# Optimization experiments

Hardware: AMD Instinct MI355X
Metric: run time of the kernel (lower is better)

The kernel has to match this reference:

```python
import jax, jax.numpy as jnp
import numpy as np

N_FEATURES = 3072
LATENT_DIM = 128
BATCH = 8192


def setup_inputs() -> dict:
    key = jax.random.key(0)
    k1, k2, k3, k4 = jax.random.split(key, 4)
    example = jax.random.normal(k1, (BATCH, N_FEATURES), dtype=jnp.float32)
    # small-ish W so C = W W^T + sigma^2 I is well conditioned
    W = jax.random.normal(k2, (N_FEATURES, LATENT_DIM), dtype=jnp.float32) * 0.05
    log_var = jax.random.normal(k3, (1,), dtype=jnp.float32) * 0.1
    training_mean = jax.random.normal(k4, (N_FEATURES,), dtype=jnp.float32)
    return {"example": example, "W": W, "log_var": log_var, "training_mean": training_mean}


def reference(example, W, log_var, training_mean):
    n = W.shape[0]
    # C = W W^T + exp(log_var) * I   -- [n, n] covariance, as in the original
    C = W @ W.T + jnp.exp(log_var[0]) * jnp.eye(n, dtype=W.dtype)
    _, logdetC = jnp.linalg.slogdet(C)
    precision = jnp.linalg.inv(C)
    res = example.reshape(-1, n) - training_mean.reshape(1, n)  # [B, n]
    # diag(res @ precision @ res^T) computed directly, avoiding the BxB matrix
    quad = jnp.einsum("bi,ij,bj->b", res, precision, res)  # [B]
    log_2pi = np.log(2.0 * np.pi).astype(np.float32)
    log_like = -0.5 * (n * log_2pi + logdetC + quad)  # [B]
    return log_like
```

## Files before the change

### kernel.cpp

```cpp
#include <hip/hip_runtime.h>
#include <hip/hip_bf16.h>

#define N_FEAT 3072
#define LATENT 128
#define LOG2PI 1.8378770664093453f

typedef __attribute__((ext_vector_type(8))) short short8;
typedef __attribute__((ext_vector_type(4))) float f32x4;

__device__ __forceinline__ unsigned short f2bf(float x) {
  unsigned int u = __float_as_uint(x);
  u += 0x7FFFu + ((u >> 16) & 1u);
  return (unsigned short)(u >> 16);
}

typedef __attribute__((address_space(1))) const void gas_void;
typedef __attribute__((address_space(3))) void las_void;
__device__ __forceinline__ void gld_lds16(const void* g, void* s) {
  __builtin_amdgcn_global_load_lds((gas_void*)g, (las_void*)s, 16, 0, 0);
}

#define GR_CHUNK 64
__global__ __launch_bounds__(256) void k_prep(const float* __restrict__ W,
                                              float* __restrict__ Mp,
                                              unsigned short* __restrict__ Wt) {
  __shared__ __align__(16) float Ws[GR_CHUNK * 128];
  int t = threadIdx.x;
  int k0 = blockIdx.x * GR_CHUNK;
  const float* src = W + (size_t)k0 * 128;
#pragma unroll
  for (int c = 0; c < 8; ++c)
    ((float4*)Ws)[t + 256 * c] = ((const float4*)src)[t + 256 * c];
  __syncthreads();
  int tr = t >> 4, tc = t & 15;
  float acc[8][8];
#pragma unroll
  for (int r = 0; r < 8; ++r)
#pragma unroll
    for (int c = 0; c < 8; ++c) acc[r][c] = 0.f;
#pragma unroll 2
  for (int k = 0; k < GR_CHUNK; ++k) {
    f32x4 a0 = *(f32x4*)&Ws[k * 128 + 8 * tr];
    f32x4 a1 = *(f32x4*)&Ws[k * 128 + 8 * tr + 4];
    f32x4 b0 = *(f32x4*)&Ws[k * 128 + 8 * tc];
    f32x4 b1 = *(f32x4*)&Ws[k * 128 + 8 * tc + 4];
    float av[8] = {a0.x, a0.y, a0.z, a0.w, a1.x, a1.y, a1.z, a1.w};
    float bv[8] = {b0.x, b0.y, b0.z, b0.w, b1.x, b1.y, b1.z, b1.w};
#pragma unroll
    for (int r = 0; r < 8; ++r)
#pragma unroll
      for (int c = 0; c < 8; ++c) acc[r][c] = fmaf(av[r], bv[c], acc[r][c]);
  }
  float* dst = Mp + (size_t)blockIdx.x * 16384 + (size_t)(8 * tr) * 128 + 8 * tc;
#pragma unroll
  for (int r = 0; r < 8; ++r) {
    *(f32x4*)(dst + r * 128) = (f32x4){acc[r][0], acc[r][1], acc[r][2], acc[r][3]};
    *(f32x4*)(dst + r * 128 + 4) = (f32x4){acc[r][4], acc[r][5], acc[r][6], acc[r][7]};
  }
  int n = t >> 1, h = t & 1;
  unsigned pk[16];
#pragma unroll
  for (int c = 0; c < 16; ++c)
    pk[c] = (unsigned)f2bf(Ws[(h * 32 + 2 * c) * 128 + n]) |
            ((unsigned)f2bf(Ws[(h * 32 + 2 * c + 1) * 128 + n]) << 16);
  uint4* wd = (uint4*)(Wt + (size_t)n * N_FEAT + k0 + h * 32);
#pragma unroll
  for (int c = 0; c < 4; ++c)
    wd[c] = make_uint4(pk[4 * c], pk[4 * c + 1], pk[4 * c + 2], pk[4 * c + 3]);
}

__global__ __launch_bounds__(256) void k_red(const float* __restrict__ Mp,
                                             float* __restrict__ M) {
  int i = blockIdx.x * 256 + threadIdx.x;
  float s = 0.f;
#pragma unroll
  for (int p = 0; p < 48; ++p) s += Mp[(size_t)p * 16384 + i];
  M[i] = s;
}

__global__ __launch_bounds__(512, 4) void k_gemm(
    const float* __restrict__ ex, const float* __restrict__ mean,
    const unsigned short* __restrict__ Wt, float* __restrict__ M,
    float* __restrict__ scal, const float* __restrict__ log_var,
    float* __restrict__ Tp, float* __restrict__ sqp, int direct) {
  __shared__ __align__(16) unsigned short As[2][32][128];
  __shared__ __align__(16) unsigned short Bs[2][128][128];
  int t = threadIdx.x;

  if (blockIdx.x == 0) {
    float* sh = (float*)&As[0][0][0];
    float* PR = sh;
    float* PC = sh + 256;
    float* DB = sh + 512;
    float* DG = sh + 514;
    float* RD = sh + 642;
    bool act = t < 256;
    int itr = t >> 4, itc = t & 15;
    float lv = log_var[0];
    float sig2 = expf(lv);
    float a[8][8];
    if (act) {
      const float* srcM = M + (size_t)(8 * itr) * 128 + 8 * itc;
#pragma unroll
      for (int r = 0; r < 8; ++r) {
        f32x4 v0 = *(const f32x4*)(srcM + r * 128);
        f32x4 v1 = *(const f32x4*)(srcM + r * 128 + 4);
        a[r][0] = v0.x; a[r][1] = v0.y; a[r][2] = v0.z; a[r][3] = v0.w;
        a[r][4] = v1.x; a[r][5] = v1.y; a[r][6] = v1.z; a[r][7] = v1.w;
      }
      if (itr == itc) {
#pragma unroll
        for (int r = 0; r < 8; ++r) a[r][r] += sig2;
      }
      if (itr == 0) {
#pragma unroll
        for (int c = 0; c < 8; ++c) PR[8 * itc + c] = a[0][c];
      }
      if (itc == 0) {
#pragma unroll
        for (int r = 0; r < 8; ++r) PC[8 * itr + r] = a[r][0];
      }
      if (t == 0) DB[0] = a[0][0];
    }
    __syncthreads();
    for (int kb = 0; kb < 16; ++kb) {
#pragma unroll
      for (int lk = 0; lk < 8; ++lk) {
        const int k = kb * 8 + lk;
        const int buf = k & 1;
        if (act) {
          float d = DB[buf];
          if (t == 0) DG[k] = d;
          float p = 1.0f / d;
          float pr[8], pc[8];
#pragma unroll
          for (int c = 0; c < 8; ++c) pr[c] = PR[buf * 128 + 8 * itc + c] * p;
#pragma unroll
          for (int r = 0; r < 8; ++r) pc[r] = PC[buf * 128 + 8 * itr + r];
#pragma unroll
          for (int r = 0; r < 8; ++r)
#pragma unroll
            for (int c = 0; c < 8; ++c) a[r][c] = fmaf(-pc[r], pr[c], a[r][c]);
          bool myrow = (itr == (k >> 3));
          bool mycol = (itc == (k >> 3));
          if (myrow) {
#pragma unroll
            for (int c = 0; c < 8; ++c) a[lk][c] = pr[c];
          }
          if (mycol) {
#pragma unroll
            for (int r = 0; r < 8; ++r) a[r][lk] = -p * pc[r];
          }
          if (myrow && mycol) a[lk][lk] = p;
          if (k + 1 < 128) {
            const int nb = buf ^ 1;
            const int nl = (lk + 1) & 7;
            const int nr = (k + 1) >> 3;
            if (itr == nr) {
#pragma unroll
              for (int c = 0; c < 8; ++c) PR[nb * 128 + 8 * itc + c] = a[nl][c];
            }
            if (itc == nr) {
#pragma unroll
              for (int r = 0; r < 8; ++r) PC[nb * 128 + 8 * itr + r] = a[r][nl];
            }
            if (itr == nr && itc == nr) DB[nb] = a[nl][nl];
          }
        }
        __syncthreads();
      }
    }
    if (act) {
      float* dst = M + (size_t)(8 * itr) * 128 + 8 * itc;
#pragma unroll
      for (int r = 0; r < 8; ++r) {
        f32x4 v0 = {a[r][0], a[r][1], a[r][2], a[r][3]};
        f32x4 v1 = {a[r][4], a[r][5], a[r][6], a[r][7]};
        *(f32x4*)(dst + r * 128) = v0;
        *(f32x4*)(dst + r * 128 + 4) = v1;
      }
    }
    float ld = 0.f;
    if (t < 128) ld = logf(DG[t]);
#pragma unroll
    for (int o = 1; o < 64; o <<= 1) ld += __shfl_xor(ld, o);
    if (t == 0) RD[0] = ld;
    if (t == 64) RD[1] = ld;
    __syncthreads();
    if (t == 0) {
      scal[0] = -0.5f * (N_FEAT * LOG2PI + (float)(N_FEAT - LATENT) * lv +
                         (RD[0] + RD[1]));
      scal[1] = expf(-lv);
    }
    return;
  }

  int gid = (int)blockIdx.x - 1;
  int half = gid >> 8;
  int rg = gid & 255;
  int r0 = rg * 32;
  const bool dual = (gid == 255);
  const int NT = dual ? 24 : 12;
  const int tg0 = dual ? 0 : half * 12;

  int lane = t & 63, w = t >> 6;

  int arow = t >> 4, ag = t & 15;
  const float* ep = ex + (size_t)(r0 + arow) * N_FEAT + (size_t)tg0 * 128 + ag * 8;
  const float* mp = mean + (size_t)tg0 * 128 + ag * 8;
  int awoff = arow * 256 + ((ag & 8) + ((ag + arow) & 7)) * 16;

  int sp = lane & 15, rl = lane >> 4;
  const unsigned short* bsrc[4];
#pragma unroll
  for (int j = 0; j < 4; ++j) {
    int n = w * 16 + j * 4 + rl;
    int s = (sp & 8) | ((sp - n) & 7);
    bsrc[j] = Wt + (size_t)n * N_FEAT + (size_t)tg0 * 128 + s * 8;
  }
  char* ldsB0 = (char*)Bs + (size_t)w * 4096;
  char* ldsB1 = (char*)Bs + 32768 + (size_t)w * 4096;

  int fr = lane & 15, fq = lane >> 4;
  int aoff0[4], aoff1[4], boff[4];
#pragma unroll
  for (int kk = 0; kk < 4; ++kk) {
    int sI = kk * 4 + fq;
    aoff0[kk] = fr * 256 + ((sI & 8) + ((sI + fr) & 7)) * 16;
    int ar1 = 16 + fr;
    aoff1[kk] = ar1 * 256 + ((sI & 8) + ((sI + ar1) & 7)) * 16;
    int n = w * 16 + fr;
    boff[kk] = n * 256 + ((sI & 8) + ((sI + n) & 7)) * 16;
  }

  f32x4 acc0 = {0.f, 0.f, 0.f, 0.f}, acc1 = {0.f, 0.f, 0.f, 0.f};
  float sq = 0.f;
  float4 e, e2, m, m2;

  auto issueA = [&](int it) {
    const float* p = ep + (size_t)it * 128;
    const float* q = mp + (size_t)it * 128;
    e  = *(const float4*)p;       e2 = *(const float4*)(p + 4);
    m  = *(const float4*)q;       m2 = *(const float4*)(q + 4);
  };
  auto issueB = [&](int it, int bufN) {
    char* d = bufN ? ldsB1 : ldsB0;
#pragma unroll
    for (int j = 0; j < 4; ++j)
      gld_lds16(bsrc[j] + (size_t)it * 128, d + j * 1024);
  };
  auto packA = [&](int bufN) {
    float r0_ = e.x - m.x,   r1_ = e.y - m.y,   r2_ = e.z - m.z,   r3_ = e.w - m.w;
    float r4_ = e2.x - m2.x, r5_ = e2.y - m2.y, r6_ = e2.z - m2.z, r7_ = e2.w - m2.w;
    sq = fmaf(r0_, r0_, sq); sq = fmaf(r1_, r1_, sq);
    sq = fmaf(r2_, r2_, sq); sq = fmaf(r3_, r3_, sq);
    sq = fmaf(r4_, r4_, sq); sq = fmaf(r5_, r5_, sq);
    sq = fmaf(r6_, r6_, sq); sq = fmaf(r7_, r7_, sq);
    uint4 pa;
    pa.x = (unsigned)f2bf(r0_) | ((unsigned)f2bf(r1_) << 16);
    pa.y = (unsigned)f2bf(r2_) | ((unsigned)f2bf(r3_) << 16);
    pa.z = (unsigned)f2bf(r4_) | ((unsigned)f2bf(r5_) << 16);
    pa.w = (unsigned)f2bf(r6_) | ((unsigned)f2bf(r7_) << 16);
    *(uint4*)((char*)As + bufN * 8192 + awoff) = pa;
  };
  auto mma = [&](int bufN) {
    char* Ab = (char*)As + bufN * 8192;
    char* Bb = (char*)Bs + bufN * 32768;
#pragma unroll
    for (int kk = 0; kk < 4; ++kk) {
      short8 a0 = *(const short8*)(Ab + aoff0[kk]);
      short8 a1 = *(const short8*)(Ab + aoff1[kk]);
      short8 b  = *(const short8*)(Bb + boff[kk]);
      acc0 = __builtin_amdgcn_mfma_f32_16x16x32_bf16(a0, b, acc0, 0, 0, 0);
      acc1 = __builtin_amdgcn_mfma_f32_16x16x32_bf16(a1, b, acc1, 0, 0, 0);
    }
  };

  issueA(0);
  __builtin_amdgcn_sched_barrier(0);
  issueB(0, 0);
  packA(0);
  asm volatile("s_waitcnt lgkmcnt(0)" ::: "memory");
  __builtin_amdgcn_s_barrier();
  __builtin_amdgcn_sched_barrier(0);

  for (int it = 0; it < NT - 1; ++it) {
    const int buf = it & 1;
    issueA(it + 1);
    __builtin_amdgcn_sched_barrier(0);
    issueB(it + 1, buf ^ 1);
    asm volatile("s_waitcnt vmcnt(8)" ::: "memory");
    __builtin_amdgcn_sched_barrier(0);
    mma(buf);
    packA(buf ^ 1);
    asm volatile("s_waitcnt lgkmcnt(0)" ::: "memory");
    __builtin_amdgcn_s_barrier();
    __builtin_amdgcn_sched_barrier(0);
  }
  asm volatile("s_waitcnt vmcnt(0)" ::: "memory");
  __builtin_amdgcn_sched_barrier(0);
  mma((NT - 1) & 1);

  sq += __shfl_xor(sq, 1); sq += __shfl_xor(sq, 2);
  sq += __shfl_xor(sq, 4); sq += __shfl_xor(sq, 8);

  if (direct) {
    if (ag == 0) sqp[half * 8192 + r0 + arow] = sq;
    float* tp = Tp + (size_t)half * 1048576 +
                (size_t)(r0 + fq * 4) * 128 + w * 16 + fr;
#pragma unroll
    for (int ii = 0; ii < 4; ++ii) {
      tp[(size_t)ii * 128] = acc0[ii];
      tp[(size_t)ii * 128 + 2048] = acc1[ii];
    }
    if (dual) {
      float* z = Tp + 1048576 + (size_t)r0 * 128;
      for (int i = t; i < 1024; i += 512) ((f32x4*)z)[i] = (f32x4){0, 0, 0, 0};
      if (t < 32) sqp[8192 + r0 + t] = 0.f;
    }
  } else {
    if (ag == 0) atomicAdd(&sqp[r0 + arow], sq);
    float* tp = Tp + (size_t)(r0 + fq * 4) * 128 + w * 16 + fr;
#pragma unroll
    for (int ii = 0; ii < 4; ++ii) {
      atomicAdd(tp + (size_t)ii * 128, acc0[ii]);
      atomicAdd(tp + (size_t)ii * 128 + 2048, acc1[ii]);
    }
  }
}

__global__ __launch_bounds__(256) void k_epi(const float* __restrict__ Tp,
                                             const float* __restrict__ sqp,
                                             const float* __restrict__ Minv,
                                             const float* __restrict__ scal,
                                             float* __restrict__ out, int two) {
  __shared__ __align__(16) float Ts[32][132];
  __shared__ float rs[32];
  int t = threadIdx.x;
  int r0 = blockIdx.x * 32;
  int sr = t >> 3, sseg = t & 7;
  const float* tp0 = Tp + (size_t)(r0 + sr) * 128 + sseg * 16;
#pragma unroll
  for (int c = 0; c < 4; ++c) {
    float4 v0 = *(const float4*)(tp0 + c * 4);
    if (two) {
      float4 v1 = *(const float4*)(tp0 + 1048576 + c * 4);
      v0.x += v1.x; v0.y += v1.y; v0.z += v1.z; v0.w += v1.w;
    }
    *(f32x4*)&Ts[sr][sseg * 16 + c * 4] = (f32x4){v0.x, v0.y, v0.z, v0.w};
  }
  if (t < 32) rs[t] = two ? (sqp[r0 + t] + sqp[8192 + r0 + t]) : sqp[r0 + t];
  __syncthreads();

  int rp = t >> 4, cg = t & 15;
  int ra = 2 * rp, rb = ra + 1;
  int c0 = cg * 8;
  float ya[8] = {0, 0, 0, 0, 0, 0, 0, 0};
  float yb[8] = {0, 0, 0, 0, 0, 0, 0, 0};
#pragma unroll 4
  for (int j = 0; j < 128; ++j) {
    float tav = Ts[ra][j];
    float tbv = Ts[rb][j];
    float4 v0 = *(const float4*)(Minv + j * LATENT + c0);
    float4 v1 = *(const float4*)(Minv + j * LATENT + c0 + 4);
    ya[0] = fmaf(tav, v0.x, ya[0]); ya[1] = fmaf(tav, v0.y, ya[1]);
    ya[2] = fmaf(tav, v0.z, ya[2]); ya[3] = fmaf(tav, v0.w, ya[3]);
    ya[4] = fmaf(tav, v1.x, ya[4]); ya[5] = fmaf(tav, v1.y, ya[5]);
    ya[6] = fmaf(tav, v1.z, ya[6]); ya[7] = fmaf(tav, v1.w, ya[7]);
    yb[0] = fmaf(tbv, v0.x, yb[0]); yb[1] = fmaf(tbv, v0.y, yb[1]);
    yb[2] = fmaf(tbv, v0.z, yb[2]); yb[3] = fmaf(tbv, v0.w, yb[3]);
    yb[4] = fmaf(tbv, v1.x, yb[4]); yb[5] = fmaf(tbv, v1.y, yb[5]);
    yb[6] = fmaf(tbv, v1.z, yb[6]); yb[7] = fmaf(tbv, v1.w, yb[7]);
  }
  float q0 = 0.f, q1 = 0.f;
#pragma unroll
  for (int c = 0; c < 8; ++c) {
    q0 = fmaf(ya[c], Ts[ra][c0 + c], q0);
    q1 = fmaf(yb[c], Ts[rb][c0 + c], q1);
  }
  q0 += __shfl_xor(q0, 1); q0 += __shfl_xor(q0, 2);
  q0 += __shfl_xor(q0, 4); q0 += __shfl_xor(q0, 8);
  q1 += __shfl_xor(q1, 1); q1 += __shfl_xor(q1, 2);
  q1 += __shfl_xor(q1, 4); q1 += __shfl_xor(q1, 8);
  if (cg == 0) {
    float cc = scal[0], is2 = scal[1];
    out[r0 + ra] = cc - 0.5f * is2 * (rs[ra] - q0);
    out[r0 + rb] = cc - 0.5f * is2 * (rs[rb] - q1);
  }
}

extern "C" void kernel_launch(void* const* d_in, const int* in_sizes, int n_in,
                              void* d_out, int out_size, void* d_ws, size_t ws_size,
                              hipStream_t stream) {
  (void)in_sizes; (void)n_in; (void)out_size;
  const float* ex   = (const float*)d_in[0];
  const float* W    = (const float*)d_in[1];
  const float* lv   = (const float*)d_in[2];
  const float* mean = (const float*)d_in[3];
  float* out = (float*)d_out;

  const size_t need_direct = (size_t)(16384 + 64 + 2097152 + 16384 + 196608) * 4;
  int direct = (ws_size >= need_direct) ? 1 : 0;

  float* M = (float*)d_ws;
  float* scal = M + 16384;
  float* Tp = scal + 64;
  float* sqp;
  unsigned short* Wt;
  if (direct) {
    sqp = Tp + 2097152;
    Wt = (unsigned short*)(sqp + 16384);
  } else {
    sqp = Tp + 1048576;
    Wt = (unsigned short*)(sqp + 8192);
  }
  float* Mp = Tp;

  k_prep<<<48, 256, 0, stream>>>(W, Mp, Wt);
  k_red<<<64, 256, 0, stream>>>(Mp, M);
  if (!direct)
    hipMemsetAsync(Tp, 0, (size_t)(1048576 + 8192) * sizeof(float), stream);
  k_gemm<<<512, 512, 0, stream>>>(ex, mean, Wt, M, scal, lv, Tp, sqp, direct);
  k_epi<<<256, 256, 0, stream>>>(Tp, sqp, M, scal, out, direct ? 1 : 0);
}
```

Baseline: 212.7 us.

## Fuse all stages into one cooperative kernel with grid syncs and split-K A pipelining

Merges the prep, reduction, inverse/GEMM and epilogue kernels into a single cooperative launch that separates stages with grid-wide barriers, removing per-launch overheads and gaps between kernels. The GEMM main loop is also restructured into a manually unrolled two-stage register pipeline for the activation loads. The dual-half special block is dropped, since block 0 now does the inverse and then the last row-group half. Separate-kernel fallbacks are kept for when the cooperative launch fails. The risks are grid.sync cost across 512 blocks and the occupancy needed for a cooperative launch of 512x512 threads.

```diff
diff --git a/kernel.cpp b/kernel.cpp
--- a/kernel.cpp
+++ b/kernel.cpp
@@ -1,5 +1,8 @@
 #include <hip/hip_runtime.h>
 #include <hip/hip_bf16.h>
+#include <hip/hip_cooperative_groups.h>
+
+namespace cg = cooperative_groups;
 
 #define N_FEAT 3072
 #define LATENT 128
@@ -20,189 +23,183 @@
   __builtin_amdgcn_global_load_lds((gas_void*)g, (las_void*)s, 16, 0, 0);
 }
 
-#define GR_CHUNK 64
-__global__ __launch_bounds__(256) void k_prep(const float* __restrict__ W,
-                                              float* __restrict__ Mp,
-                                              unsigned short* __restrict__ Wt) {
-  __shared__ __align__(16) float Ws[GR_CHUNK * 128];
-  int t = threadIdx.x;
-  int k0 = blockIdx.x * GR_CHUNK;
-  const float* src = W + (size_t)k0 * 128;
-#pragma unroll
-  for (int c = 0; c < 8; ++c)
-    ((float4*)Ws)[t + 256 * c] = ((const float4*)src)[t + 256 * c];
+__device__ void prep_body(char* smem, int bid, int t, const float* W,
+                          float* Mp, unsigned short* Wt) {
+  float* Ws = (float*)smem;
+  int k0 = bid * 64;
+  if (t < 256) {
+    const float* src = W + (size_t)k0 * 128;
+#pragma unroll
+    for (int c = 0; c < 8; ++c)
+      ((float4*)Ws)[t + 256 * c] = ((const float4*)src)[t + 256 * c];
+  }
   __syncthreads();
-  int tr = t >> 4, tc = t & 15;
-  float acc[8][8];
-#pragma unroll
-  for (int r = 0; r < 8; ++r)
-#pragma unroll
-    for (int c = 0; c < 8; ++c) acc[r][c] = 0.f;
+  if (t < 256) {
+    int tr = t >> 4, tc = t & 15;
+    float acc[8][8];
+#pragma unroll
+    for (int r = 0; r < 8; ++r)
+#pragma unroll
+      for (int c = 0; c < 8; ++c) acc[r][c] = 0.f;
 #pragma unroll 2
-  for (int k = 0; k < GR_CHUNK; ++k) {
-    f32x4 a0 = *(f32x4*)&Ws[k * 128 + 8 * tr];
-    f32x4 a1 = *(f32x4*)&Ws[k * 128 + 8 * tr + 4];
-    f32x4 b0 = *(f32x4*)&Ws[k * 128 + 8 * tc];
-    f32x4 b1 = *(f32x4*)&Ws[k * 128 + 8 * tc + 4];
-    float av[8] = {a0.x, a0.y, a0.z, a0.w, a1.x, a1.y, a1.z, a1.w};
-    float bv[8] = {b0.x, b0.y, b0.z, b0.w, b1.x, b1.y, b1.z, b1.w};
-#pragma unroll
-    for (int r = 0; r < 8; ++r)
-#pragma unroll
-      for (int c = 0; c < 8; ++c) acc[r][c] = fmaf(av[r], bv[c], acc[r][c]);
-  }
-  float* dst = Mp + (size_t)blockIdx.x * 16384 + (size_t)(8 * tr) * 128 + 8 * tc;
-#pragma unroll
-  for (int r = 0; r < 8; ++r) {
-    *(f32x4*)(dst + r * 128) = (f32x4){acc[r][0], acc[r][1], acc[r][2], acc[r][3]};
-    *(f32x4*)(dst + r * 128 + 4) = (f32x4){acc[r][4], acc[r][5], acc[r][6], acc[r][7]};
-  }
-  int n = t >> 1, h = t & 1;
-  unsigned pk[16];
-#pragma unroll
-  for (int c = 0; c < 16; ++c)
-    pk[c] = (unsigned)f2bf(Ws[(h * 32 + 2 * c) * 128 + n]) |
-            ((unsigned)f2bf(Ws[(h * 32 + 2 * c + 1) * 128 + n]) << 16);
-  uint4* wd = (uint4*)(Wt + (size_t)n * N_FEAT + k0 + h * 32);
-#pragma unroll
-  for (int c = 0; c < 4; ++c)
-    wd[c] = make_uint4(pk[4 * c], pk[4 * c + 1], pk[4 * c + 2], pk[4 * c + 3]);
-}
-
-__global__ __launch_bounds__(256) void k_red(const float* __restrict__ Mp,
-                                             float* __restrict__ M) {
-  int i = blockIdx.x * 256 + threadIdx.x;
-  float s = 0.f;
-#pragma unroll
-  for (int p = 0; p < 48; ++p) s += Mp[(size_t)p * 16384 + i];
-  M[i] = s;
-}
-
-__global__ __launch_bounds__(512, 4) void k_gemm(
-    const float* __restrict__ ex, const float* __restrict__ mean,
-    const unsigned short* __restrict__ Wt, float* __restrict__ M,
-    float* __restrict__ scal, const float* __restrict__ log_var,
-    float* __restrict__ Tp, float* __restrict__ sqp, int direct) {
-  __shared__ __align__(16) unsigned short As[2][32][128];
-  __shared__ __align__(16) unsigned short Bs[2][128][128];
-  int t = threadIdx.x;
-
-  if (blockIdx.x == 0) {
-    float* sh = (float*)&As[0][0][0];
-    float* PR = sh;
-    float* PC = sh + 256;
-    float* DB = sh + 512;
-    float* DG = sh + 514;
-    float* RD = sh + 642;
-    bool act = t < 256;
-    int itr = t >> 4, itc = t & 15;
-    float lv = log_var[0];
-    float sig2 = expf(lv);
-    float a[8][8];
-    if (act) {
-      const float* srcM = M + (size_t)(8 * itr) * 128 + 8 * itc;
-#pragma unroll
-      for (int r = 0; r < 8; ++r) {
-        f32x4 v0 = *(const f32x4*)(srcM + r * 128);
-        f32x4 v1 = *(const f32x4*)(srcM + r * 128 + 4);
-        a[r][0] = v0.x; a[r][1] = v0.y; a[r][2] = v0.z; a[r][3] = v0.w;
-        a[r][4] = v1.x; a[r][5] = v1.y; a[r][6] = v1.z; a[r][7] = v1.w;
+    for (int k = 0; k < 64; ++k) {
+      f32x4 a0 = *(f32x4*)&Ws[k * 128 + 8 * tr];
+      f32x4 a1 = *(f32x4*)&Ws[k * 128 + 8 * tr + 4];
+      f32x4 b0 = *(f32x4*)&Ws[k * 128 + 8 * tc];
+      f32x4 b1 = *(f32x4*)&Ws[k * 128 + 8 * tc + 4];
+      float av[8] = {a0.x, a0.y, a0.z, a0.w, a1.x, a1.y, a1.z, a1.w};
+      float bv[8] = {b0.x, b0.y, b0.z, b0.w, b1.x, b1.y, b1.z, b1.w};
+#pragma unroll
+      for (int r = 0; r < 8; ++r)
+#pragma unroll
+        for (int c = 0; c < 8; ++c) acc[r][c] = fmaf(av[r], bv[c], acc[r][c]);
+    }
+    float* dst = Mp + (size_t)bid * 16384 + (size_t)(8 * tr) * 128 + 8 * tc;
+#pragma unroll
+    for (int r = 0; r < 8; ++r) {
+      *(f32x4*)(dst + r * 128) =
+          (f32x4){acc[r][0], acc[r][1], acc[r][2], acc[r][3]};
+      *(f32x4*)(dst + r * 128 + 4) =
+          (f32x4){acc[r][4], acc[r][5], acc[r][6], acc[r][7]};
+    }
+    int n = t >> 1, h = t & 1;
+    unsigned pk[16];
+#pragma unroll
+    for (int c = 0; c < 16; ++c)
+      pk[c] = (unsigned)f2bf(Ws[(h * 32 + 2 * c) * 128 + n]) |
+              ((unsigned)f2bf(Ws[(h * 32 + 2 * c + 1) * 128 + n]) << 16);
+    uint4* wd = (uint4*)(Wt + (size_t)n * N_FEAT + k0 + h * 32);
+#pragma unroll
+    for (int c = 0; c < 4; ++c)
+      wd[c] = make_uint4(pk[4 * c], pk[4 * c + 1], pk[4 * c + 2], pk[4 * c + 3]);
+  }
+}
+
+__device__ void red_body(int bid, int t, const float* Mp, float* M) {
+  if (bid < 64 && t < 256) {
+    int i = bid * 256 + t;
+    float s = 0.f;
+#pragma unroll
+    for (int p = 0; p < 48; ++p) s += Mp[(size_t)p * 16384 + i];
+    M[i] = s;
+  }
+}
+
+__device__ void inverse_body(char* smem, int t, float* M, float* scal,
+                             const float* log_var) {
+  float* sh = (float*)smem;
+  float* PR = sh;
+  float* PC = sh + 256;
+  float* DB = sh + 512;
+  float* DG = sh + 514;
+  float* RD = sh + 642;
+  bool act = t < 256;
+  int itr = t >> 4, itc = t & 15;
+  float lv = log_var[0];
+  float sig2 = expf(lv);
+  float a[8][8];
+  if (act) {
+    const float* srcM = M + (size_t)(8 * itr) * 128 + 8 * itc;
+#pragma unroll
+    for (int r = 0; r < 8; ++r) {
+      f32x4 v0 = *(const f32x4*)(srcM + r * 128);
+      f32x4 v1 = *(const f32x4*)(srcM + r * 128 + 4);
+      a[r][0] = v0.x; a[r][1] = v0.y; a[r][2] = v0.z; a[r][3] = v0.w;
+      a[r][4] = v1.x; a[r][5] = v1.y; a[r][6] = v1.z; a[r][7] = v1.w;
+    }
+    if (itr == itc) {
+#pragma unroll
+      for (int r = 0; r < 8; ++r) a[r][r] += sig2;
+    }
+    if (itr == 0) {
+#pragma unroll
+      for (int c = 0; c < 8; ++c) PR[8 * itc + c] = a[0][c];
+    }
+    if (itc == 0) {
+#pragma unroll
+      for (int r = 0; r < 8; ++r) PC[8 * itr + r] = a[r][0];
+    }
+    if (t == 0) DB[0] = a[0][0];
+  }
+  __syncthreads();
+  for (int kb = 0; kb < 16; ++kb) {
+#pragma unroll
+    for (int lk = 0; lk < 8; ++lk) {
+      const int k = kb * 8 + lk;
+      const int buf = k & 1;
+      if (act) {
+        float d = DB[buf];
+        if (t == 0) DG[k] = d;
+        float p = 1.0f / d;
+        float pr[8], pc[8];
+#pragma unroll
+        for (int c = 0; c < 8; ++c) pr[c] = PR[buf * 128 + 8 * itc + c] * p;
+#pragma unroll
+        for (int r = 0; r < 8; ++r) pc[r] = PC[buf * 128 + 8 * itr + r];
+#pragma unroll
+        for (int r = 0; r < 8; ++r)
+#pragma unroll
+          for (int c = 0; c < 8; ++c) a[r][c] = fmaf(-pc[r], pr[c], a[r][c]);
+        bool myrow = (itr == (k >> 3));
+        bool mycol = (itc == (k >> 3));
+        if (myrow) {
+#pragma unroll
+          for (int c = 0; c < 8; ++c) a[lk][c] = pr[c];
+        }
+        if (mycol) {
+#pragma unroll
+          for (int r = 0; r < 8; ++r) a[r][lk] = -p * pc[r];
+        }
+        if (myrow && mycol) a[lk][lk] = p;
+        if (k + 1 < 128) {
+          const int nb = buf ^ 1;
+          const int nl = (lk + 1) & 7;
+          const int nr = (k + 1) >> 3;
+          if (itr == nr) {
+#pragma unroll
+            for (int c = 0; c < 8; ++c) PR[nb * 128 + 8 * itc + c] = a[nl][c];
+          }
+          if (itc == nr) {
+#pragma unroll
+            for (int r = 0; r < 8; ++r) PC[nb * 128 + 8 * itr + r] = a[r][nl];
+          }
+          if (itr == nr && itc == nr) DB[nb] = a[nl][nl];
+        }
       }
-      if (itr == itc) {
-#pragma unroll
-        for (int r = 0; r < 8; ++r) a[r][r] += sig2;
-      }
-      if (itr == 0) {
-#pragma unroll
-        for (int c = 0; c < 8; ++c) PR[8 * itc + c] = a[0][c];
-      }
-      if (itc == 0) {
-#pragma unroll
-        for (int r = 0; r < 8; ++r) PC[8 * itr + r] = a[r][0];
-      }
-      if (t == 0) DB[0] = a[0][0];
-    }
-    __syncthreads();
-    for (int kb = 0; kb < 16; ++kb) {
-#pragma unroll
-      for (int lk = 0; lk < 8; ++lk) {
-        const int k = kb * 8 + lk;
-        const int buf = k & 1;
-        if (act) {
-          float d = DB[buf];
-          if (t == 0) DG[k] = d;
-          float p = 1.0f / d;
-          float pr[8], pc[8];
-#pragma unroll
-          for (int c = 0; c < 8; ++c) pr[c] = PR[buf * 128 + 8 * itc + c] * p;
-#pragma unroll
-          for (int r = 0; r < 8; ++r) pc[r] = PC[buf * 128 + 8 * itr + r];
-#pragma unroll
-          for (int r = 0; r < 8; ++r)
-#pragma unroll
-            for (int c = 0; c < 8; ++c) a[r][c] = fmaf(-pc[r], pr[c], a[r][c]);
-          bool myrow = (itr == (k >> 3));
-          bool mycol = (itc == (k >> 3));
-          if (myrow) {
-#pragma unroll
-            for (int c = 0; c < 8; ++c) a[lk][c] = pr[c];
-          }
-          if (mycol) {
-#pragma unroll
-            for (int r = 0; r < 8; ++r) a[r][lk] = -p * pc[r];
-          }
-          if (myrow && mycol) a[lk][lk] = p;
-          if (k + 1 < 128) {
-            const int nb = buf ^ 1;
-            const int nl = (lk + 1) & 7;
-            const int nr = (k + 1) >> 3;
-            if (itr == nr) {
-#pragma unroll
-              for (int c = 0; c < 8; ++c) PR[nb * 128 + 8 * itc + c] = a[nl][c];
-            }
-            if (itc == nr) {
-#pragma unroll
-              for (int r = 0; r < 8; ++r) PC[nb * 128 + 8 * itr + r] = a[r][nl];
-            }
-            if (itr == nr && itc == nr) DB[nb] = a[nl][nl];
-          }
-        }
-        __syncthreads();
-      }
-    }
-    if (act) {
-      float* dst = M + (size_t)(8 * itr) * 128 + 8 * itc;
-#pragma unroll
-      for (int r = 0; r < 8; ++r) {
-        f32x4 v0 = {a[r][0], a[r][1], a[r][2], a[r][3]};
-        f32x4 v1 = {a[r][4], a[r][5], a[r][6], a[r][7]};
-        *(f32x4*)(dst + r * 128) = v0;
-        *(f32x4*)(dst + r * 128 + 4) = v1;
-      }
-    }
-    float ld = 0.f;
-    if (t < 128) ld = logf(DG[t]);
-#pragma unroll
-    for (int o = 1; o < 64; o <<= 1) ld += __shfl_xor(ld, o);
-    if (t == 0) RD[0] = ld;
-    if (t == 64) RD[1] = ld;
-    __syncthreads();
-    if (t == 0) {
-      scal[0] = -0.5f * (N_FEAT * LOG2PI + (float)(N_FEAT - LATENT) * lv +
-                         (RD[0] + RD[1]));
-      scal[1] = expf(-lv);
-    }
-    return;
-  }
-
-  int gid = (int)blockIdx.x - 1;
-  int half = gid >> 8;
-  int rg = gid & 255;
+      __syncthreads();
+    }
+  }
+  if (act) {
+    float* dst = M + (size_t)(8 * itr) * 128 + 8 * itc;
+#pragma unroll
+    for (int r = 0; r < 8; ++r) {
+      f32x4 v0 = {a[r][0], a[r][1], a[r][2], a[r][3]};
+      f32x4 v1 = {a[r][4], a[r][5], a[r][6], a[r][7]};
+      *(f32x4*)(dst + r * 128) = v0;
+      *(f32x4*)(dst + r * 128 + 4) = v1;
+    }
+  }
+  float ld = 0.f;
+  if (t < 128) ld = logf(DG[t]);
+#pragma unroll
+  for (int o = 1; o < 64; o <<= 1) ld += __shfl_xor(ld, o);
+  if (t == 0) RD[0] = ld;
+  if (t == 64) RD[1] = ld;
+  __syncthreads();
+  if (t == 0) {
+    scal[0] = -0.5f * (N_FEAT * LOG2PI + (float)(N_FEAT - LATENT) * lv +
+                       (RD[0] + RD[1]));
+    scal[1] = expf(-lv);
+  }
+}
+
+__device__ void gemm_body(char* smem, int rg, int half, int t,
+                          const float* ex, const float* mean,
+                          const unsigned short* Wt, float* Tp, float* sqp) {
+  char* As = smem;
+  char* Bs = smem + 16384;
   int r0 = rg * 32;
-  const bool dual = (gid == 255);
-  const int NT = dual ? 24 : 12;
-  const int tg0 = dual ? 0 : half * 12;
-
+  int tg0 = half * 12;
   int lane = t & 63, w = t >> 6;
 
   int arow = t >> 4, ag = t & 15;
@@ -218,8 +215,8 @@
     int s = (sp & 8) | ((sp - n) & 7);
     bsrc[j] = Wt + (size_t)n * N_FEAT + (size_t)tg0 * 128 + s * 8;
   }
-  char* ldsB0 = (char*)Bs + (size_t)w * 4096;
-  char* ldsB1 = (char*)Bs + 32768 + (size_t)w * 4096;
+  char* ldsB0 = Bs + (size_t)w * 4096;
+  char* ldsB1 = Bs + 32768 + (size_t)w * 4096;
 
   int fr = lane & 15, fq = lane >> 4;
   int aoff0[4], aoff1[4], boff[4];
@@ -235,21 +232,23 @@
 
   f32x4 acc0 = {0.f, 0.f, 0.f, 0.f}, acc1 = {0.f, 0.f, 0.f, 0.f};
   float sq = 0.f;
-  float4 e, e2, m, m2;
-
-  auto issueA = [&](int it) {
+  float4 eA, eA2, mA, mA2;
+  float4 eB, eB2, mB, mB2;
+
+  auto loadS0 = [&](int it) {
     const float* p = ep + (size_t)it * 128;
     const float* q = mp + (size_t)it * 128;
-    e  = *(const float4*)p;       e2 = *(const float4*)(p + 4);
-    m  = *(const float4*)q;       m2 = *(const float4*)(q + 4);
+    eA = *(const float4*)p;  eA2 = *(const float4*)(p + 4);
+    mA = *(const float4*)q;  mA2 = *(const float4*)(q + 4);
   };
-  auto issueB = [&](int it, int bufN) {
-    char* d = bufN ? ldsB1 : ldsB0;
-#pragma unroll
-    for (int j = 0; j < 4; ++j)
-      gld_lds16(bsrc[j] + (size_t)it * 128, d + j * 1024);
+  auto loadS1 = [&](int it) {
+    const float* p = ep + (size_t)it * 128;
+    const float* q = mp + (size_t)it * 128;
+    eB = *(const float4*)p;  eB2 = *(const float4*)(p + 4);
+    mB = *(const float4*)q;  mB2 = *(const float4*)(q + 4);
   };
-  auto packA = [&](int bufN) {
+  auto packS = [&](const float4& e, const float4& e2, const float4& m,
+                   const float4& m2, int bufN) {
     float r0_ = e.x - m.x,   r1_ = e.y - m.y,   r2_ = e.z - m.z,   r3_ = e.w - m.w;
     float r4_ = e2.x - m2.x, r5_ = e2.y - m2.y, r6_ = e2.z - m2.z, r7_ = e2.w - m2.w;
     sq = fmaf(r0_, r0_, sq); sq = fmaf(r1_, r1_, sq);
@@ -261,11 +260,17 @@
     pa.y = (unsigned)f2bf(r2_) | ((unsigned)f2bf(r3_) << 16);
     pa.z = (unsigned)f2bf(r4_) | ((unsigned)f2bf(r5_) << 16);
     pa.w = (unsigned)f2bf(r6_) | ((unsigned)f2bf(r7_) << 16);
-    *(uint4*)((char*)As + bufN * 8192 + awoff) = pa;
+    *(uint4*)(As + bufN * 8192 + awoff) = pa;
+  };
+  auto issueB = [&](int it, int bufN) {
+    char* d = bufN ? ldsB1 : ldsB0;
+#pragma unroll
+    for (int j = 0; j < 4; ++j)
+      gld_lds16(bsrc[j] + (size_t)it * 128, d + j * 1024);
   };
   auto mma = [&](int bufN) {
-    char* Ab = (char*)As + bufN * 8192;
-    char* Bb = (char*)Bs + bufN * 32768;
+    char* Ab = As + bufN * 8192;
+    char* Bb = Bs + bufN * 32768;
 #pragma unroll
     for (int kk = 0; kk < 4; ++kk) {
       short8 a0 = *(const short8*)(Ab + aoff0[kk]);
@@ -276,150 +281,220 @@
     }
   };
 
-  issueA(0);
+  loadS0(0);
+  loadS1(1);
   __builtin_amdgcn_sched_barrier(0);
   issueB(0, 0);
-  packA(0);
+  packS(eA, eA2, mA, mA2, 0);
+  loadS0(2);
   asm volatile("s_waitcnt lgkmcnt(0)" ::: "memory");
   __builtin_amdgcn_s_barrier();
   __builtin_amdgcn_sched_barrier(0);
 
-  for (int it = 0; it < NT - 1; ++it) {
-    const int buf = it & 1;
-    issueA(it + 1);
-    __builtin_amdgcn_sched_barrier(0);
-    issueB(it + 1, buf ^ 1);
+#pragma unroll
+  for (int j = 0; j < 5; ++j) {
+    const int it0 = 2 * j;
+    issueB(it0 + 1, 1);
     asm volatile("s_waitcnt vmcnt(8)" ::: "memory");
     __builtin_amdgcn_sched_barrier(0);
-    mma(buf);
-    packA(buf ^ 1);
+    mma(0);
+    packS(eB, eB2, mB, mB2, 1);
+    loadS1(it0 + 3 < 12 ? it0 + 3 : 11);
     asm volatile("s_waitcnt lgkmcnt(0)" ::: "memory");
     __builtin_amdgcn_s_barrier();
     __builtin_amdgcn_sched_barrier(0);
-  }
+    issueB(it0 + 2, 0);
+    asm volatile("s_waitcnt vmcnt(8)" ::: "memory");
+    __builtin_amdgcn_sched_barrier(0);
+    mma(1);
+    packS(eA, eA2, mA, mA2, 0);
+    loadS0(it0 + 4 < 12 ? it0 + 4 : 11);
+    asm volatile("s_waitcnt lgkmcnt(0)" ::: "memory");
+    __builtin_amdgcn_s_barrier();
+    __builtin_amdgcn_sched_barrier(0);
+  }
+  issueB(11, 1);
+  asm volatile("s_waitcnt vmcnt(8)" ::: "memory");
+  __builtin_amdgcn_sched_barrier(0);
+  mma(0);
+  packS(eB, eB2, mB, mB2, 1);
+  asm volatile("s_waitcnt lgkmcnt(0)" ::: "memory");
+  __builtin_amdgcn_s_barrier();
+  __builtin_amdgcn_sched_barrier(0);
   asm volatile("s_waitcnt vmcnt(0)" ::: "memory");
   __builtin_amdgcn_sched_barrier(0);
-  mma((NT - 1) & 1);
+  mma(1);
 
   sq += __shfl_xor(sq, 1); sq += __shfl_xor(sq, 2);
   sq += __shfl_xor(sq, 4); sq += __shfl_xor(sq, 8);
-
-  if (direct) {
-    if (ag == 0) sqp[half * 8192 + r0 + arow] = sq;
-    float* tp = Tp + (size_t)half * 1048576 +
-                (size_t)(r0 + fq * 4) * 128 + w * 16 + fr;
-#pragma unroll
-    for (int ii = 0; ii < 4; ++ii) {
-      tp[(size_t)ii * 128] = acc0[ii];
-      tp[(size_t)ii * 128 + 2048] = acc1[ii];
-    }
-    if (dual) {
-      float* z = Tp + 1048576 + (size_t)r0 * 128;
-      for (int i = t; i < 1024; i += 512) ((f32x4*)z)[i] = (f32x4){0, 0, 0, 0};
-      if (t < 32) sqp[8192 + r0 + t] = 0.f;
-    }
+  if (ag == 0) sqp[half * 8192 + r0 + arow] = sq;
+
+  float* tp = Tp + (size_t)half * 1048576 +
+              (size_t)(r0 + fq * 4) * 128 + w * 16 + fr;
+#pragma unroll
+  for (int ii = 0; ii < 4; ++ii) {
+    tp[(size_t)ii * 128] = acc0[ii];
+    tp[(size_t)ii * 128 + 2048] = acc1[ii];
+  }
+}
+
+__device__ void epi_body(char* smem, int bid, int t, const float* Tp,
+                         const float* sqp, const float* Minv,
+                         const float* scal, float* out) {
+  if (bid >= 256) return;
+  float (*Ts)[132] = (float(*)[132])smem;
+  float* rs = (float*)(smem + 32 * 132 * 4);
+  int r0 = bid * 32;
+  if (t < 256) {
+    int sr = t >> 3, sseg = t & 7;
+    const float* tp0 = Tp + (size_t)(r0 + sr) * 128 + sseg * 16;
+    const float* tp1 = tp0 + 1048576;
+#pragma unroll
+    for (int c = 0; c < 4; ++c) {
+      float4 v0 = *(const float4*)(tp0 + c * 4);
+      float4 v1 = *(const float4*)(tp1 + c * 4);
+      *(f32x4*)&Ts[sr][sseg * 16 + c * 4] =
+          (f32x4){v0.x + v1.x, v0.y + v1.y, v0.z + v1.z, v0.w + v1.w};
+    }
+    if (t < 32) rs[t] = sqp[r0 + t] + sqp[8192 + r0 + t];
+  }
+  __syncthreads();
+  if (t < 256) {
+    int rp = t >> 4, cg2 = t & 15;
+    int ra = 2 * rp, rb = ra + 1;
+    int c0 = cg2 * 8;
+    float ya[8] = {0, 0, 0, 0, 0, 0, 0, 0};
+    float yb[8] = {0, 0, 0, 0, 0, 0, 0, 0};
+#pragma unroll 4
+    for (int j = 0; j < 128; ++j) {
+      float tav = Ts[ra][j];
+      float tbv = Ts[rb][j];
+      float4 v0 = *(const float4*)(Minv + j * LATENT + c0);
+      float4 v1 = *(const float4*)(Minv + j * LATENT + c0 + 4);
+      ya[0] = fmaf(tav, v0.x, ya[0]); ya[1] = fmaf(tav, v0.y, ya[1]);
+      ya[2] = fmaf(tav, v0.z, ya[2]); ya[3] = fmaf(tav, v0.w, ya[3]);
+      ya[4] = fmaf(tav, v1.x, ya[4]); ya[5] = fmaf(tav, v1.y, ya[5]);
+      ya[6] = fmaf(tav, v1.z, ya[6]); ya[7] = fmaf(tav, v1.w, ya[7]);
+      yb[0] = fmaf(tbv, v0.x, yb[0]); yb[1] = fmaf(tbv, v0.y, yb[1]);
+      yb[2] = fmaf(tbv, v0.z, yb[2]); yb[3] = fmaf(tbv, v0.w, yb[3]);
+      yb[4] = fmaf(tbv, v1.x, yb[4]); yb[5] = fmaf(tbv, v1.y, yb[5]);
+      yb[6] = fmaf(tbv, v1.z, yb[6]); yb[7] = fmaf(tbv, v1.w, yb[7]);
+    }
+    float q0 = 0.f, q1 = 0.f;
+#pragma unroll
+    for (int c = 0; c < 8; ++c) {
+      q0 = fmaf(ya[c], Ts[ra][c0 + c], q0);
+      q1 = fmaf(yb[c], Ts[rb][c0 + c], q1);
+    }
+    q0 += __shfl_xor(q0, 1); q0 += __shfl_xor(q0, 2);
+    q0 += __shfl_xor(q0, 4); q0 += __shfl_xor(q0, 8);
+    q1 += __shfl_xor(q1, 1); q1 += __shfl_xor(q1, 2);
+    q1 += __shfl_xor(q1, 4); q1 += __shfl_xor(q1, 8);
+    if (cg2 == 0) {
+      float cc = scal[0], is2 = scal[1];
+      out[r0 + ra] = cc - 0.5f * is2 * (rs[ra] - q0);
+      out[r0 + rb] = cc - 0.5f * is2 * (rs[rb] - q1);
+    }
+  }
+}
+
+__global__ __launch_bounds__(512, 4) void k_all(
+    const float* __restrict__ ex, const float* __restrict__ W,
+    const float* __restrict__ lv, const float* __restrict__ mean,
+    float* __restrict__ M, float* __restrict__ scal, float* __restrict__ Tp,
+    float* __restrict__ sqp, unsigned short* __restrict__ Wt,
+    float* __restrict__ out) {
+  __shared__ __align__(16) char smem[81920];
+  cg::grid_group grid = cg::this_grid();
+  int bid = blockIdx.x, t = threadIdx.x;
+  float* Mp = Tp;
+
+  if (bid < 48) prep_body(smem, bid, t, W, Mp, Wt);
+  __threadfence();
+  grid.sync();
+
+  red_body(bid, t, Mp, M);
+  __threadfence();
+  grid.sync();
+
+  int rg, half;
+  if (bid == 0) {
+    inverse_body(smem, t, M, scal, lv);
+    __syncthreads();
+    rg = 255; half = 1;
   } else {
-    if (ag == 0) atomicAdd(&sqp[r0 + arow], sq);
-    float* tp = Tp + (size_t)(r0 + fq * 4) * 128 + w * 16 + fr;
-#pragma unroll
-    for (int ii = 0; ii < 4; ++ii) {
-      atomicAdd(tp + (size_t)ii * 128, acc0[ii]);
-      atomicAdd(tp + (size_t)ii * 128 + 2048, acc1[ii]);
-    }
-  }
-}
-
-__global__ __launch_bounds__(256) void k_epi(const float* __restrict__ Tp,
-                                             const float* __restrict__ sqp,
-                                             const float* __restrict__ Minv,
-                                             const float* __restrict__ scal,
-                                             float* __restrict__ out, int two) {
-  __shared__ __align__(16) float Ts[32][132];
-  __shared__ float rs[32];
-  int t = threadIdx.x;
-  int r0 = blockIdx.x * 32;
-  int sr = t >> 3, sseg = t & 7;
-  const float* tp0 = Tp + (size_t)(r0 + sr) * 128 + sseg * 16;
-#pragma unroll
-  for (int c = 0; c < 4; ++c) {
-    float4 v0 = *(const float4*)(tp0 + c * 4);
-    if (two) {
-      float4 v1 = *(const float4*)(tp0 + 1048576 + c * 4);
-      v0.x += v1.x; v0.y += v1.y; v0.z += v1.z; v0.w += v1.w;
-    }
-    *(f32x4*)&Ts[sr][sseg * 16 + c * 4] = (f32x4){v0.x, v0.y, v0.z, v0.w};
-  }
-  if (t < 32) rs[t] = two ? (sqp[r0 + t] + sqp[8192 + r0 + t]) : sqp[r0 + t];
-  __syncthreads();
-
-  int rp = t >> 4, cg = t & 15;
-  int ra = 2 * rp, rb = ra + 1;
-  int c0 = cg * 8;
-  float ya[8] = {0, 0, 0, 0, 0, 0, 0, 0};
-  float yb[8] = {0, 0, 0, 0, 0, 0, 0, 0};
-#pragma unroll 4
-  for (int j = 0; j < 128; ++j) {
-    float tav = Ts[ra][j];
-    float tbv = Ts[rb][j];
-    float4 v0 = *(const float4*)(Minv + j * LATENT + c0);
-    float4 v1 = *(const float4*)(Minv + j * LATENT + c0 + 4);
-    ya[0] = fmaf(tav, v0.x, ya[0]); ya[1] = fmaf(tav, v0.y, ya[1]);
-    ya[2] = fmaf(tav, v0.z, ya[2]); ya[3] = fmaf(tav, v0.w, ya[3]);
-    ya[4] = fmaf(tav, v1.x, ya[4]); ya[5] = fmaf(tav, v1.y, ya[5]);
-    ya[6] = fmaf(tav, v1.z, ya[6]); ya[7] = fmaf(tav, v1.w, ya[7]);
-    yb[0] = fmaf(tbv, v0.x, yb[0]); yb[1] = fmaf(tbv, v0.y, yb[1]);
-    yb[2] = fmaf(tbv, v0.z, yb[2]); yb[3] = fmaf(tbv, v0.w, yb[3]);
-    yb[4] = fmaf(tbv, v1.x, yb[4]); yb[5] = fmaf(tbv, v1.y, yb[5]);
-    yb[6] = fmaf(tbv, v1.z, yb[6]); yb[7] = fmaf(tbv, v1.w, yb[7]);
-  }
-  float q0 = 0.f, q1 = 0.f;
-#pragma unroll
-  for (int c = 0; c < 8; ++c) {
-    q0 = fmaf(ya[c], Ts[ra][c0 + c], q0);
-    q1 = fmaf(yb[c], Ts[rb][c0 + c], q1);
-  }
-  q0 += __shfl_xor(q0, 1); q0 += __shfl_xor(q0, 2);
-  q0 += __shfl_xor(q0, 4); q0 += __shfl_xor(q0, 8);
-  q1 += __shfl_xor(q1, 1); q1 += __shfl_xor(q1, 2);
-  q1 += __shfl_xor(q1, 4); q1 += __shfl_xor(q1, 8);
-  if (cg == 0) {
-    float cc = scal[0], is2 = scal[1];
-    out[r0 + ra] = cc - 0.5f * is2 * (rs[ra] - q0);
-    out[r0 + rb] = cc - 0.5f * is2 * (rs[rb] - q1);
-  }
+    int g = bid - 1;
+    rg = g & 255; half = g >> 8;
+  }
+  gemm_body(smem, rg, half, t, ex, mean, Wt, Tp, sqp);
+  __threadfence();
+  grid.sync();
+
+  epi_body(smem, bid, t, Tp, sqp, M, scal, out);
+}
+
+__global__ __launch_bounds__(256) void k_prep_s(const float* __restrict__ W,
+                                                float* __restrict__ Mp,
+                                                unsigned short* __restrict__ Wt) {
+  __shared__ __align__(16) char smem[32768];
+  prep_body(smem, blockIdx.x, threadIdx.x, W, Mp, Wt);
+}
+__global__ __launch_bounds__(256) void k_red_s(const float* __restrict__ Mp,
+                                               float* __restrict__ M) {
+  red_body(blockIdx.x, threadIdx.x, Mp, M);
+}
+__global__ __launch_bounds__(512, 4) void k_gemm_s(
+    const float* __restrict__ ex, const float* __restrict__ mean,
+    const unsigned short* __restrict__ Wt, float* __restrict__ M,
+    float* __restrict__ scal, const float* __restrict__ lv,
+    float* __restrict__ Tp, float* __restrict__ sqp) {
+  __shared__ __align__(16) char smem[81920];
+  int bid = blockIdx.x, t = threadIdx.x;
+  int rg, half;
+  if (bid == 0) {
+    inverse_body(smem, t, M, scal, lv);
+    __syncthreads();
+    rg = 255; half = 1;
+  } else {
+    int g = bid - 1;
+    rg = g & 255; half = g >> 8;
+  }
+  gemm_body(smem, rg, half, t, ex, mean, Wt, Tp, sqp);
+}
+__global__ __launch_bounds__(256) void k_epi_s(
+    const float* __restrict__ Tp, const float* __restrict__ sqp,
+    const float* __restrict__ Minv, const float* __restrict__ scal,
+    float* __restrict__ out) {
+  __shared__ __align__(16) char smem[17024];
+  epi_body(smem, blockIdx.x, threadIdx.x, Tp, sqp, Minv, scal, out);
 }
 
 extern "C" void kernel_launch(void* const* d_in, const int* in_sizes, int n_in,
                               void* d_out, int out_size, void* d_ws, size_t ws_size,
                               hipStream_t stream) {
-  (void)in_sizes; (void)n_in; (void)out_size;
+  (void)in_sizes; (void)n_in; (void)out_size; (void)ws_size;
   const float* ex   = (const float*)d_in[0];
   const float* W    = (const float*)d_in[1];
   const float* lv   = (const float*)d_in[2];
   const float* mean = (const float*)d_in[3];
   float* out = (float*)d_out;
 
-  const size_t need_direct = (size_t)(16384 + 64 + 2097152 + 16384 + 196608) * 4;
-  int direct = (ws_size >= need_direct) ? 1 : 0;
-
   float* M = (float*)d_ws;
   float* scal = M + 16384;
   float* Tp = scal + 64;
-  float* sqp;
-  unsigned short* Wt;
-  if (direct) {
-    sqp = Tp + 2097152;
-    Wt = (unsigned short*)(sqp + 16384);
-  } else {
-    sqp = Tp + 1048576;
-    Wt = (unsigned short*)(sqp + 8192);
-  }
-  float* Mp = Tp;
-
-  k_prep<<<48, 256, 0, stream>>>(W, Mp, Wt);
-  k_red<<<64, 256, 0, stream>>>(Mp, M);
-  if (!direct)
-    hipMemsetAsync(Tp, 0, (size_t)(1048576 + 8192) * sizeof(float), stream);
-  k_gemm<<<512, 512, 0, stream>>>(ex, mean, Wt, M, scal, lv, Tp, sqp, direct);
-  k_epi<<<256, 256, 0, stream>>>(Tp, sqp, M, scal, out, direct ? 1 : 0);
-}
+  float* sqp = Tp + 2097152;
+  unsigned short* Wt = (unsigned short*)(sqp + 16384);
+
+  void* kargs[] = {(void*)&ex, (void*)&W, (void*)&lv, (void*)&mean,
+                   (void*)&M,  (void*)&scal, (void*)&Tp, (void*)&sqp,
+                   (void*)&Wt, (void*)&out};
+  hipError_t err = hipLaunchCooperativeKernel((const void*)k_all, dim3(512),
+                                              dim3(512), kargs, 0, stream);
+  if (err != hipSuccess) {
+    (void)hipGetLastError();
+    k_prep_s<<<48, 256, 0, stream>>>(W, Tp, Wt);
+    k_red_s<<<64, 256, 0, stream>>>(Tp, M);
+    k_gemm_s<<<512, 512, 0, stream>>>(ex, mean, Wt, M, scal, lv, Tp, sqp);
+    k_epi_s<<<256, 256, 0, stream>>>(Tp, sqp, M, scal, out);
+  }
+}
```

Result: slower. 725.1 us (+240.9%).
